# Kernel optimization log

Hardware: AMD Instinct MI355X
Metric: run time of the kernel (lower is better)

The kernel has to match this reference:

```python
import jax, jax.numpy as jnp
import numpy as np

B, S, D = 4, 4096, 64

def setup_inputs() -> dict:
    key = jax.random.key(0)
    k1, k2 = jax.random.split(key)
    query = jax.random.normal(k1, (B, S, D), dtype=jnp.float32)
    value = jax.random.normal(k2, (B, S, D), dtype=jnp.float32)
    return {"query": query, "value": value}

def reference(query, value):
    # score = Q @ V^T  -> [B, Sq, Skv]  (note: value acts as both key and value; no 1/sqrt(d) scaling)
    score = jnp.einsum("bqd,bkd->bqk", query, value)
    attn_weights = jax.nn.softmax(score, axis=-1)
    context = jnp.einsum("bqk,bkd->bqd", attn_weights, value)
    return (context, attn_weights)
```

## Files before the change

### kernel.cpp

```cpp
#include <hip/hip_runtime.h>

#define BB 4
#define SS 4096
#define DD 64
#define QB 32
#define TK 32
#define NS 4
#define SV 72
#define SVT 40
#define SP 72

typedef _Float16 h16;
typedef h16 half4_t __attribute__((ext_vector_type(4)));
typedef h16 half8_t __attribute__((ext_vector_type(8)));
typedef float f32x4 __attribute__((ext_vector_type(4)));

struct __align__(16) LdsBufs {
    h16 Vhi[NS][TK * SV];
    h16 Vlo[NS][TK * SV];
    h16 VTr[NS][DD * SVT];
    h16 Pl[8][16 * SP];
};
static_assert(sizeof(LdsBufs) <= 80 * 1024, "need 2 blocks/CU");

struct StReg { f32x4 v[4]; };

__device__ __forceinline__ void stage_load(StReg& r, const float* Vb, int it, int t) {
    const int c16 = t & 15;
    const int rg  = t >> 4;
    const f32x4* Vg = (const f32x4*)(Vb + ((size_t)it * (NS * TK) + rg * 4) * DD);
#pragma unroll
    for (int i = 0; i < 4; ++i) r.v[i] = Vg[i * 16 + c16];
}

__device__ __forceinline__ void stage_write(const StReg& r, LdsBufs& L, int t, bool with_vt) {
    const int c16 = t & 15;
    const int rg  = t >> 4;
    const int ts  = rg >> 3;
    const int r0  = (rg & 7) * 4;
    half4_t hh[4];
#pragma unroll
    for (int i = 0; i < 4; ++i) {
        f32x4 v = r.v[i];
        half4_t hi, lo;
#pragma unroll
        for (int j = 0; j < 4; ++j) {
            float x = v[j];
            h16 h = (h16)x;
            hi[j] = h;
            lo[j] = (h16)(x - (float)h);
        }
        hh[i] = hi;
        *(half4_t*)&L.Vhi[ts][(r0 + i) * SV + c16 * 4] = hi;
        *(half4_t*)&L.Vlo[ts][(r0 + i) * SV + c16 * 4] = lo;
    }
    if (with_vt) {
#pragma unroll
        for (int j = 0; j < 4; ++j) {
            half4_t col;
#pragma unroll
            for (int i = 0; i < 4; ++i) col[i] = hh[i][j];
            *(half4_t*)&L.VTr[ts][(c16 * 4 + j) * SVT + r0] = col;
        }
    }
}

__device__ __forceinline__ void scores(const LdsBufs& L, int kq, int qi, int quad,
                                       const half8_t* qhi, const half8_t* qlo,
                                       f32x4* sc) {
    sc[0] = (f32x4){0.f, 0.f, 0.f, 0.f};
    sc[1] = (f32x4){0.f, 0.f, 0.f, 0.f};
#pragma unroll
    for (int ks = 0; ks < 2; ++ks) {
#pragma unroll
        for (int mt = 0; mt < 2; ++mt) {
            half8_t ahi = *(const half8_t*)&L.Vhi[kq][(mt * 16 + qi) * SV + ks * 32 + quad * 8];
            half8_t alo = *(const half8_t*)&L.Vlo[kq][(mt * 16 + qi) * SV + ks * 32 + quad * 8];
            sc[mt] = __builtin_amdgcn_mfma_f32_16x16x32_f16(ahi, qhi[ks], sc[mt], 0, 0, 0);
            sc[mt] = __builtin_amdgcn_mfma_f32_16x16x32_f16(ahi, qlo[ks], sc[mt], 0, 0, 0);
            sc[mt] = __builtin_amdgcn_mfma_f32_16x16x32_f16(alo, qhi[ks], sc[mt], 0, 0, 0);
        }
    }
}

__global__ __launch_bounds__(512, 4) void attn_fused(const float* __restrict__ Q,
                                                     const float* __restrict__ V,
                                                     float* __restrict__ ctx,
                                                     float* __restrict__ attn) {
    __shared__ LdsBufs L;
    const int t     = threadIdx.x;
    const int w     = t >> 6;
    const int lane  = t & 63;
    const int qi    = lane & 15;
    const int quad  = lane >> 4;
    const int qgrp  = w & 1;
    const int kq    = w >> 1;
    const int b     = blockIdx.y;
    const int qb    = blockIdx.x * QB + qgrp * 16;

    const float* Vb   = V + (size_t)b * SS * DD;
    const float* Qrow = Q + ((size_t)b * SS + qb + qi) * DD;

    half8_t qhi[2], qlo[2];
#pragma unroll
    for (int ks = 0; ks < 2; ++ks) {
        f32x4 a = *(const f32x4*)(Qrow + ks * 32 + quad * 8);
        f32x4 c = *(const f32x4*)(Qrow + ks * 32 + quad * 8 + 4);
#pragma unroll
        for (int j = 0; j < 4; ++j) {
            float x = a[j];
            h16 h = (h16)x;
            qhi[ks][j] = h;
            qlo[ks][j] = (h16)(x - (float)h);
            float y = c[j];
            h16 g = (h16)y;
            qhi[ks][j + 4] = g;
            qlo[ks][j + 4] = (h16)(y - (float)g);
        }
    }

    float mrun = -1e30f, lrun = 0.f;
    f32x4 oc[4];
#pragma unroll
    for (int mt = 0; mt < 4; ++mt) oc[mt] = (f32x4){0.f, 0.f, 0.f, 0.f};

    const int NIT = SS / (NS * TK);
    StReg r;
    stage_load(r, Vb, 0, t);

    for (int it = 0; it < NIT; ++it) {
        __syncthreads();
        stage_write(r, L, t, true);
        __syncthreads();
        if (it + 1 < NIT) stage_load(r, Vb, it + 1, t);

        f32x4 sc[2];
        scores(L, kq, qi, quad, qhi, qlo, sc);

        float tmax = -1e30f;
#pragma unroll
        for (int mt = 0; mt < 2; ++mt)
#pragma unroll
            for (int r4 = 0; r4 < 4; ++r4) tmax = fmaxf(tmax, sc[mt][r4]);
        tmax = fmaxf(tmax, __shfl_xor(tmax, 16));
        tmax = fmaxf(tmax, __shfl_xor(tmax, 32));
        float mn    = fmaxf(mrun, tmax);
        float alpha = __expf(mrun - mn);
        float psum  = 0.f;
        half4_t pv[2];
#pragma unroll
        for (int mt = 0; mt < 2; ++mt)
#pragma unroll
            for (int r4 = 0; r4 < 4; ++r4) {
                float p = __expf(sc[mt][r4] - mn);
                psum += p;
                pv[mt][r4] = (h16)p;
            }
        psum += __shfl_xor(psum, 16);
        psum += __shfl_xor(psum, 32);
        lrun = lrun * alpha + psum;
        mrun = mn;
#pragma unroll
        for (int mt = 0; mt < 2; ++mt)
            *(half4_t*)&L.Pl[w][qi * SP + mt * 16 + quad * 4] = pv[mt];
#pragma unroll
        for (int mt = 0; mt < 4; ++mt) oc[mt] *= alpha;

        half8_t bp = *(const half8_t*)&L.Pl[w][qi * SP + quad * 8];
#pragma unroll
        for (int mt = 0; mt < 4; ++mt) {
            half8_t av = *(const half8_t*)&L.VTr[kq][(mt * 16 + qi) * SVT + quad * 8];
            oc[mt] = __builtin_amdgcn_mfma_f32_16x16x32_f16(av, bp, oc[mt], 0, 0, 0);
        }
    }

    stage_load(r, Vb, 0, t);

    __syncthreads();
    {
        float* buf  = (float*)&L;
        float* mine = buf + t * 18;
        mine[0] = mrun;
        mine[1] = lrun;
#pragma unroll
        for (int mt = 0; mt < 4; ++mt)
#pragma unroll
            for (int r4 = 0; r4 < 4; ++r4) mine[2 + mt * 4 + r4] = oc[mt][r4];
        __syncthreads();
        float mf = -1e30f;
#pragma unroll
        for (int k2 = 0; k2 < 4; ++k2)
            mf = fmaxf(mf, buf[((k2 * 2 + qgrp) * 64 + lane) * 18]);
        float lf = 0.f;
        f32x4 on[4];
#pragma unroll
        for (int mt = 0; mt < 4; ++mt) on[mt] = (f32x4){0.f, 0.f, 0.f, 0.f};
#pragma unroll
        for (int k2 = 0; k2 < 4; ++k2) {
            const float* po = buf + ((k2 * 2 + qgrp) * 64 + lane) * 18;
            float e = __expf(po[0] - mf);
            lf += po[1] * e;
#pragma unroll
            for (int mt = 0; mt < 4; ++mt)
#pragma unroll
                for (int r4 = 0; r4 < 4; ++r4) on[mt][r4] += po[2 + mt * 4 + r4] * e;
        }
        mrun = mf;
        lrun = lf;
#pragma unroll
        for (int mt = 0; mt < 4; ++mt) oc[mt] = on[mt];
    }

    const float invl = 1.f / lrun;

    if (kq == 0) {
        float* crow = ctx + ((size_t)b * SS + qb + qi) * DD;
#pragma unroll
        for (int mt = 0; mt < 4; ++mt) {
            f32x4 cv;
#pragma unroll
            for (int r4 = 0; r4 < 4; ++r4) cv[r4] = oc[mt][r4] * invl;
            *(f32x4*)&crow[mt * 16 + quad * 4] = cv;
        }
    }

    const float moff = mrun + __logf(lrun);
    float* arow = attn + ((size_t)b * SS + qb + qi) * SS;
    for (int it = 0; it < NIT; ++it) {
        __syncthreads();
        stage_write(r, L, t, false);
        __syncthreads();
        if (it + 1 < NIT) stage_load(r, Vb, it + 1, t);

        f32x4 sc[2];
        scores(L, kq, qi, quad, qhi, qlo, sc);
        const int kbase = it * (NS * TK) + kq * TK;
#pragma unroll
        for (int mt = 0; mt < 2; ++mt) {
            f32x4 wv;
#pragma unroll
            for (int r4 = 0; r4 < 4; ++r4) wv[r4] = __expf(sc[mt][r4] - moff);
            *(f32x4*)&arow[kbase + mt * 16 + quad * 4] = wv;
        }
    }
}

extern "C" void kernel_launch(void* const* d_in, const int* in_sizes, int n_in,
                              void* d_out, int out_size, void* d_ws, size_t ws_size,
                              hipStream_t stream) {
    const float* Q = (const float*)d_in[0];
    const float* V = (const float*)d_in[1];
    float* ctx  = (float*)d_out;
    float* attn = (float*)d_out + (size_t)BB * SS * DD;
    attn_fused<<<dim3(SS / QB, BB), 512, 0, stream>>>(Q, V, ctx, attn);
}
```

Before: 377.2 us.

## Precompute split-fp16 V tiles in a prep kernel and DMA them into LDS

```diff
diff --git a/kernel.cpp b/kernel.cpp
--- a/kernel.cpp
+++ b/kernel.cpp
@@ -9,39 +9,57 @@
 #define SV 72
 #define SVT 40
 #define SP 72
+#define NIT (SS / (NS * TK))
 
 typedef _Float16 h16;
 typedef h16 half4_t __attribute__((ext_vector_type(4)));
 typedef h16 half8_t __attribute__((ext_vector_type(8)));
 typedef float f32x4 __attribute__((ext_vector_type(4)));
 
-struct __align__(16) LdsBufs {
+struct __align__(16) VTile {
     h16 Vhi[NS][TK * SV];
     h16 Vlo[NS][TK * SV];
     h16 VTr[NS][DD * SVT];
+};
+
+struct __align__(16) LdsBufs {
+    VTile T;
     h16 Pl[8][16 * SP];
 };
+static_assert(sizeof(VTile) == 57344, "image size");
 static_assert(sizeof(LdsBufs) <= 80 * 1024, "need 2 blocks/CU");
 
-struct StReg { f32x4 v[4]; };
-
-__device__ __forceinline__ void stage_load(StReg& r, const float* Vb, int it, int t) {
-    const int c16 = t & 15;
-    const int rg  = t >> 4;
-    const f32x4* Vg = (const f32x4*)(Vb + ((size_t)it * (NS * TK) + rg * 4) * DD);
-#pragma unroll
-    for (int i = 0; i < 4; ++i) r.v[i] = Vg[i * 16 + c16];
-}
-
-__device__ __forceinline__ void stage_write(const StReg& r, LdsBufs& L, int t, bool with_vt) {
+typedef __attribute__((address_space(3))) uint32_t lds_u32;
+typedef const __attribute__((address_space(1))) uint32_t gl_u32;
+
+__device__ __forceinline__ void stage_tile(const char* g, char* l, int t,
+                                           int nfull, bool tail_half) {
+#pragma unroll
+    for (int i = 0; i < nfull; ++i) {
+        const int off = (i * 512 + t) * 16;
+        __builtin_amdgcn_global_load_lds((gl_u32*)(g + off), (lds_u32*)(l + off), 16, 0, 0);
+    }
+    if (tail_half && t < 256) {
+        const int off = (nfull * 512 + t) * 16;
+        __builtin_amdgcn_global_load_lds((gl_u32*)(g + off), (lds_u32*)(l + off), 16, 0, 0);
+    }
+}
+
+__global__ __launch_bounds__(512) void prep_v(const float* __restrict__ V,
+                                              VTile* __restrict__ W) {
+    const int t   = threadIdx.x;
+    const int it  = blockIdx.x;
+    const int b   = blockIdx.y;
     const int c16 = t & 15;
     const int rg  = t >> 4;
     const int ts  = rg >> 3;
     const int r0  = (rg & 7) * 4;
+    VTile* w = W + (size_t)b * NIT + it;
+    const f32x4* Vg = (const f32x4*)(V + ((size_t)b * SS + (size_t)it * (NS * TK) + rg * 4) * DD);
     half4_t hh[4];
 #pragma unroll
     for (int i = 0; i < 4; ++i) {
-        f32x4 v = r.v[i];
+        f32x4 v = Vg[i * 16 + c16];
         half4_t hi, lo;
 #pragma unroll
         for (int j = 0; j < 4; ++j) {
@@ -51,17 +69,15 @@
             lo[j] = (h16)(x - (float)h);
         }
         hh[i] = hi;
-        *(half4_t*)&L.Vhi[ts][(r0 + i) * SV + c16 * 4] = hi;
-        *(half4_t*)&L.Vlo[ts][(r0 + i) * SV + c16 * 4] = lo;
-    }
-    if (with_vt) {
-#pragma unroll
-        for (int j = 0; j < 4; ++j) {
-            half4_t col;
-#pragma unroll
-            for (int i = 0; i < 4; ++i) col[i] = hh[i][j];
-            *(half4_t*)&L.VTr[ts][(c16 * 4 + j) * SVT + r0] = col;
-        }
+        *(half4_t*)&w->Vhi[ts][(r0 + i) * SV + c16 * 4] = hi;
+        *(half4_t*)&w->Vlo[ts][(r0 + i) * SV + c16 * 4] = lo;
+    }
+#pragma unroll
+    for (int j = 0; j < 4; ++j) {
+        half4_t col;
+#pragma unroll
+        for (int i = 0; i < 4; ++i) col[i] = hh[i][j];
+        *(half4_t*)&w->VTr[ts][(c16 * 4 + j) * SVT + r0] = col;
     }
 }
 
@@ -74,8 +90,8 @@
     for (int ks = 0; ks < 2; ++ks) {
 #pragma unroll
         for (int mt = 0; mt < 2; ++mt) {
-            half8_t ahi = *(const half8_t*)&L.Vhi[kq][(mt * 16 + qi) * SV + ks * 32 + quad * 8];
-            half8_t alo = *(const half8_t*)&L.Vlo[kq][(mt * 16 + qi) * SV + ks * 32 + quad * 8];
+            half8_t ahi = *(const half8_t*)&L.T.Vhi[kq][(mt * 16 + qi) * SV + ks * 32 + quad * 8];
+            half8_t alo = *(const half8_t*)&L.T.Vlo[kq][(mt * 16 + qi) * SV + ks * 32 + quad * 8];
             sc[mt] = __builtin_amdgcn_mfma_f32_16x16x32_f16(ahi, qhi[ks], sc[mt], 0, 0, 0);
             sc[mt] = __builtin_amdgcn_mfma_f32_16x16x32_f16(ahi, qlo[ks], sc[mt], 0, 0, 0);
             sc[mt] = __builtin_amdgcn_mfma_f32_16x16x32_f16(alo, qhi[ks], sc[mt], 0, 0, 0);
@@ -84,7 +100,7 @@
 }
 
 __global__ __launch_bounds__(512, 4) void attn_fused(const float* __restrict__ Q,
-                                                     const float* __restrict__ V,
+                                                     const VTile* __restrict__ W,
                                                      float* __restrict__ ctx,
                                                      float* __restrict__ attn) {
     __shared__ LdsBufs L;
@@ -98,7 +114,7 @@
     const int b     = blockIdx.y;
     const int qb    = blockIdx.x * QB + qgrp * 16;
 
-    const float* Vb   = V + (size_t)b * SS * DD;
+    const VTile* Wb   = W + (size_t)b * NIT;
     const float* Qrow = Q + ((size_t)b * SS + qb + qi) * DD;
 
     half8_t qhi[2], qlo[2];
@@ -124,15 +140,10 @@
 #pragma unroll
     for (int mt = 0; mt < 4; ++mt) oc[mt] = (f32x4){0.f, 0.f, 0.f, 0.f};
 
-    const int NIT = SS / (NS * TK);
-    StReg r;
-    stage_load(r, Vb, 0, t);
-
     for (int it = 0; it < NIT; ++it) {
         __syncthreads();
-        stage_write(r, L, t, true);
-        __syncthreads();
-        if (it + 1 < NIT) stage_load(r, Vb, it + 1, t);
+        stage_tile((const char*)(Wb + it), (char*)&L.T, t, 7, false);
+        __syncthreads();
 
         f32x4 sc[2];
         scores(L, kq, qi, quad, qhi, qlo, sc);
@@ -169,12 +180,10 @@
         half8_t bp = *(const half8_t*)&L.Pl[w][qi * SP + quad * 8];
 #pragma unroll
         for (int mt = 0; mt < 4; ++mt) {
-            half8_t av = *(const half8_t*)&L.VTr[kq][(mt * 16 + qi) * SVT + quad * 8];
+            half8_t av = *(const half8_t*)&L.T.VTr[kq][(mt * 16 + qi) * SVT + quad * 8];
             oc[mt] = __builtin_amdgcn_mfma_f32_16x16x32_f16(av, bp, oc[mt], 0, 0, 0);
         }
     }
-
-    stage_load(r, Vb, 0, t);
 
     __syncthreads();
     {
@@ -228,9 +237,8 @@
     float* arow = attn + ((size_t)b * SS + qb + qi) * SS;
     for (int it = 0; it < NIT; ++it) {
         __syncthreads();
-        stage_write(r, L, t, false);
-        __syncthreads();
-        if (it + 1 < NIT) stage_load(r, Vb, it + 1, t);
+        stage_tile((const char*)(Wb + it), (char*)&L.T, t, 4, true);
+        __syncthreads();
 
         f32x4 sc[2];
         scores(L, kq, qi, quad, qhi, qlo, sc);
@@ -240,7 +248,7 @@
             f32x4 wv;
 #pragma unroll
             for (int r4 = 0; r4 < 4; ++r4) wv[r4] = __expf(sc[mt][r4] - moff);
-            *(f32x4*)&arow[kbase + mt * 16 + quad * 4] = wv;
+            __builtin_nontemporal_store(wv, (f32x4*)&arow[kbase + mt * 16 + quad * 4]);
         }
     }
 }
@@ -252,5 +260,7 @@
     const float* V = (const float*)d_in[1];
     float* ctx  = (float*)d_out;
     float* attn = (float*)d_out + (size_t)BB * SS * DD;
-    attn_fused<<<dim3(SS / QB, BB), 512, 0, stream>>>(Q, V, ctx, attn);
-}
+    VTile* W = (VTile*)d_ws;
+    prep_v<<<dim3(NIT, BB), 512, 0, stream>>>(V, W);
+    attn_fused<<<dim3(SS / QB, BB), 512, 0, stream>>>(Q, W, ctx, attn);
+}
```

Result: no change. 371.8 us (-1.4%).
